# Kernel tuning notes

Hardware: AMD Instinct MI355X
Metric: run time of the kernel (lower is better)

## Reference

```python
import jax, jax.numpy as jnp
import numpy as np

B, V, C = 8192, 512, 16  # batch, num_variables, constraints per variable
N1 = V + 1  # augmented with bias column


def setup_inputs() -> dict:
    key = jax.random.key(0)
    k1, k2, k3 = jax.random.split(key, 3)
    preds = jax.random.normal(k1, (B, V), dtype=jnp.float32)
    # Acyclic structure: variable v's constraints only reference earlier
    # variables (columns < v) plus the bias column (column V).
    cols = jnp.arange(N1)[None, :]              # [1, N1]
    vids = jnp.arange(V)[:, None]               # [V, 1]
    mask = ((cols < vids) | (cols == V)).astype(jnp.float32)[:, None, :]  # [V,1,N1]
    scale = 0.1
    pos_mats = jax.random.normal(k2, (V, C, N1), dtype=jnp.float32) * scale * mask
    neg_mats = jax.random.normal(k3, (V, C, N1), dtype=jnp.float32) * scale * mask
    return {"preds": preds, "pos_mats": pos_mats, "neg_mats": neg_mats}


def reference(preds, pos_mats, neg_mats):
    # Augment preds with a ones column (bias), as in the original __call__.
    b = preds.shape[0]
    p0 = jnp.concatenate([preds, jnp.ones((b, 1), preds.dtype)], axis=1)  # [B, N1]
    var_ids = jnp.arange(pos_mats.shape[0])

    def step(p, xs):
        pm, nm, v = xs  # pm, nm: [C, N1]
        # apply_matrix: (preds * matrix).sum(-1) with max / min reduction over C
        lower = jnp.einsum('bn,cn->bc', p, pm).max(axis=1)  # [B]
        upper = jnp.einsum('bn,cn->bc', p, nm).min(axis=1)  # [B]
        # get_final_x_correction: clamp prediction into [lower, upper]
        corrected = jnp.minimum(jnp.maximum(p[:, v], lower), upper)
        p = p.at[:, v].set(corrected)
        return p, None

    pf, _ = jax.lax.scan(step, p0, (pos_mats, neg_mats, var_ids))
    return pf[:, : preds.shape[1]]
```

## Files before the change

kernel.cpp:

```cpp
#include <hip/hip_runtime.h>

#define BATCH 8192
#define V 512
#define N1 513
#define KCH 16
#define NCHUNKS 32
#define RB 32
#define NT 1024
#define PKS 520
#define SJP 772

typedef __bf16 bf16_t;
typedef bf16_t bf16x8 __attribute__((ext_vector_type(8)));
typedef float f32x4 __attribute__((ext_vector_type(4)));
typedef float f32x2 __attribute__((ext_vector_type(2)));

#define EPP 4194304ull
#define DV_OFF (EPP * 2ull)
#define BV_OFF (DV_OFF + 1048576ull)

__device__ __forceinline__ f32x4 mfma16(bf16x8 a, bf16x8 b, f32x4 c) {
    return __builtin_amdgcn_mfma_f32_16x16x32_bf16(a, b, c, 0, 0, 0);
}

__device__ __forceinline__ float bcast_lane(float x, int l) {
    return __int_as_float(__builtin_amdgcn_readlane(__float_as_int(x), l));
}

__device__ __forceinline__ float dpp_xor1_max(float x) {
    const int xi = __float_as_int(x);
    const float o = __int_as_float(
        __builtin_amdgcn_update_dpp(xi, xi, 0xB1, 0xF, 0xF, false));
    return fmaxf(x, o);
}

__global__ __launch_bounds__(256)
void repack_all(const float* __restrict__ pos, const float* __restrict__ neg,
                bf16_t* __restrict__ Mhi, float* __restrict__ Dv,
                float* __restrict__ Bv)
{
    __shared__ float bufP[256 * 17];
    __shared__ float bufN[256 * 17];
    const int bx = blockIdx.x;
    if (bx < 496) {
        const int cc  = (bx >> 4) + 1;
        const int kb  = bx & 15;
        const int nkb = (cc + 1) >> 1;
        if (kb >= nkb) return;
        const int klen = 16 * cc;
        const size_t base = 16384ull * (size_t)((cc * cc) / 4) + (size_t)kb * 16384ull;
        for (int e = threadIdx.x; e < 16384; e += 256) {
            const int t = e >> 9, s = (e >> 3) & 63, jj = e & 7;
            const int c = s & 15, q = s >> 4;
            const int v = cc * 16 + (t >> 1);
            const int k = kb * 32 + 8 * q + jj;
            const float* src = (t & 1) ? neg : pos;
            float x = (k < klen) ? src[(size_t)(v * 16 + c) * N1 + k] : 0.0f;
            if (t & 1) x = -x;
            Mhi[base + e] = (bf16_t)x;
        }
    } else {
        const int cc = bx - 496;
        for (int idx = threadIdx.x; idx < 4096; idx += 256) {
            const int r = idx >> 4, kk = idx & 15;
            const size_t row = (size_t)(cc * 256 + r);
            bufP[r * 17 + kk] = pos[row * N1 + cc * 16 + kk];
            bufN[r * 17 + kk] = neg[row * N1 + cc * 16 + kk];
        }
        __syncthreads();
        for (int idx = threadIdx.x; idx < 8192; idx += 256) {
            const int vl = idx >> 9, j = idx & 511;
            const int vlo = j >> 5, c = j & 15;
            const int m = (j >> 4) & 1;
            const float x = (m ? bufN : bufP)[(vlo * 16 + c) * 17 + vl];
            Dv[(size_t)cc * 8192 + idx] = m ? -x : x;
        }
        for (int j = threadIdx.x; j < 512; j += 256) {
            const int vlo = j >> 5, c = j & 15;
            const int m = (j >> 4) & 1;
            const float* src = m ? neg : pos;
            const float x = src[(size_t)(cc * 256 + vlo * 16 + c) * N1 + V];
            Bv[(size_t)cc * 512 + j] = m ? -x : x;
        }
    }
}

__global__ __launch_bounds__(NT, 4)
void shield_fused(const float* __restrict__ preds,
                  const bf16_t* __restrict__ Mhi,
                  const float* __restrict__ Dv, const float* __restrict__ Bv,
                  float* __restrict__ out)
{
    __shared__ bf16_t Phi[RB * PKS];
    __shared__ float  S[RB * SJP];

    const int tid  = threadIdx.x;
    const int b0   = blockIdx.x * RB;
    const int lane = tid & 63;
    const int w    = tid >> 6;
    const int cq   = lane & 15;
    const int q    = lane >> 4;
    const int rp0  = w * 2;

    {
        const int r = tid >> 5, seg = tid & 31;
        const float* prow = preds + (size_t)(b0 + r) * V + seg * 16;
        #pragma unroll
        for (int k = 0; k < 16; k += 4) {
            const float4 p4 = *(const float4*)(prow + k);
            const int n = seg * 16 + k;
            Phi[r * PKS + n + 0] = (bf16_t)p4.x;
            Phi[r * PKS + n + 1] = (bf16_t)p4.y;
            Phi[r * PKS + n + 2] = (bf16_t)p4.z;
            Phi[r * PKS + n + 3] = (bf16_t)p4.w;
        }
    }

    int tJ[2], sct[2];
    #pragma unroll
    for (int tt = 0; tt < 2; ++tt) {
        tJ[tt]  = ((2 * w + tt) << 4) + cq;
        sct[tt] = 12 * (tJ[tt] >> 3) + (tJ[tt] & 7);
    }
    const int aoff0 = cq * PKS + 8 * q;
    const int aoff1 = (16 + cq) * PKS + 8 * q;

    f32x4 acc[2][2];
    #pragma unroll
    for (int tt = 0; tt < 2; ++tt) {
        const float b = Bv[tJ[tt]];
        acc[0][tt] = f32x4{b, b, b, b};
        acc[1][tt] = f32x4{b, b, b, b};
    }

    #pragma unroll 1
    for (int cc = 0; cc < NCHUNKS; ++cc) {
        const int v0 = cc * 16;
        const int  ccn  = cc + 1;
        const bool hasN = ccn < NCHUNKS;
        const int  nkbN = hasN ? ((ccn + 1) >> 1) : 0;
        const bf16_t* phN = Mhi + 16384ull * (size_t)((ccn * ccn) / 4)
                          + (size_t)lane * 8 + (size_t)(2 * w) * 512;

        #pragma unroll
        for (int tt = 0; tt < 2; ++tt)
            #pragma unroll
            for (int reg = 0; reg < 4; ++reg) {
                S[(4 * q + reg) * SJP + sct[tt]]      = acc[0][tt][reg];
                S[(16 + 4 * q + reg) * SJP + sct[tt]] = acc[1][tt][reg];
            }
        __syncthreads();

        f32x2 s2[8];
        {
            const float* sp = &S[rp0 * SJP + 12 * lane];
            const float4 a0 = *(const float4*)(sp);
            const float4 a1 = *(const float4*)(sp + 4);
            const float4 c0 = *(const float4*)(sp + SJP);
            const float4 c1 = *(const float4*)(sp + SJP + 4);
            s2[0] = f32x2{a0.x, c0.x}; s2[1] = f32x2{a0.y, c0.y};
            s2[2] = f32x2{a0.z, c0.z}; s2[3] = f32x2{a0.w, c0.w};
            s2[4] = f32x2{a1.x, c1.x}; s2[5] = f32x2{a1.y, c1.y};
            s2[6] = f32x2{a1.z, c1.z}; s2[7] = f32x2{a1.w, c1.w};
        }

        const bf16x8 poA0 = *(const bf16x8*)(Phi + rp0 * PKS + v0);
        const bf16x8 poA1 = *(const bf16x8*)(Phi + rp0 * PKS + v0 + 8);
        const bf16x8 poB0 = *(const bf16x8*)(Phi + (rp0 + 1) * PKS + v0);
        const bf16x8 poB1 = *(const bf16x8*)(Phi + (rp0 + 1) * PKS + v0 + 8);

        if (hasN) {
            #pragma unroll
            for (int tt = 0; tt < 2; ++tt) {
                const float b = Bv[(ccn << 9) + tJ[tt]];
                acc[0][tt] = f32x4{b, b, b, b};
                acc[1][tt] = f32x4{b, b, b, b};
            }
        }

        #pragma unroll
        for (int vl = 0; vl < KCH; ++vl) {
            const int vcur = v0 + vl;
            const bool doKb = hasN && (vl < nkbN - 1);

            bf16x8 fa0, fa1, fb0, fb1;
            if (doKb) {
                const int k0 = vl * 32;
                fa0 = *(const bf16x8*)(Phi + aoff0 + k0);
                fa1 = *(const bf16x8*)(Phi + aoff1 + k0);
                const bf16_t* pb = phN + (size_t)k0 * 512;
                fb0 = *(const bf16x8*)(pb);
                fb1 = *(const bf16x8*)(pb + 512);
            }

            float dv[8];
            {
                const float* dp = Dv + ((size_t)vcur << 9) + 8 * lane;
                const float4 d0 = *(const float4*)(dp);
                const float4 d1 = *(const float4*)(dp + 4);
                dv[0]=d0.x; dv[1]=d0.y; dv[2]=d0.z; dv[3]=d0.w;
                dv[4]=d1.x; dv[5]=d1.y; dv[6]=d1.z; dv[7]=d1.w;
            }
            const float po_[2] = {
                (float)(vl < 8 ? poA0[vl & 7] : poA1[vl & 7]),
                (float)(vl < 8 ? poB0[vl & 7] : poB1[vl & 7])
            };

            float red[2];
            #pragma unroll
            for (int r = 0; r < 2; ++r) {
                const float m0 = fmaxf(fmaxf(s2[0][r], s2[1][r]), s2[2][r]);
                const float m1 = fmaxf(fmaxf(s2[3][r], s2[4][r]), s2[5][r]);
                const float m2 = fmaxf(s2[6][r], s2[7][r]);
                const float mxr = fmaxf(fmaxf(m0, m1), m2);
                red[r] = dpp_xor1_max(mxr);
            }
            float pc[2];
            #pragma unroll
            for (int r = 0; r < 2; ++r) {
                const float lw  = bcast_lane(red[r], 4 * vl);
                const float nup = bcast_lane(red[r], 4 * vl + 2);
                pc[r] = fminf(fmaxf(po_[r], lw), -nup);
            }
            if (lane == 4 * vl) {
                Phi[rp0 * PKS + vcur]       = (bf16_t)pc[0];
                Phi[(rp0 + 1) * PKS + vcur] = (bf16_t)pc[1];
            }
            const f32x2 pcv = {pc[0], pc[1]};
            #pragma unroll
            for (int jj = 0; jj < 8; ++jj) {
                const f32x2 dsp = {dv[jj], dv[jj]};
                s2[jj] = __builtin_elementwise_fma(dsp, pcv, s2[jj]);
            }

            if (doKb) {
                acc[0][0] = mfma16(fa0, fb0, acc[0][0]);
                acc[1][0] = mfma16(fa1, fb0, acc[1][0]);
                acc[0][1] = mfma16(fa0, fb1, acc[0][1]);
                acc[1][1] = mfma16(fa1, fb1, acc[1][1]);
            }
        }

        __syncthreads();

        if (hasN) {
            const int k0 = (nkbN - 1) * 32;
            const bf16x8 fa0 = *(const bf16x8*)(Phi + aoff0 + k0);
            const bf16x8 fa1 = *(const bf16x8*)(Phi + aoff1 + k0);
            const bf16_t* pb = phN + (size_t)k0 * 512;
            const bf16x8 fb0 = *(const bf16x8*)(pb);
            const bf16x8 fb1 = *(const bf16x8*)(pb + 512);
            acc[0][0] = mfma16(fa0, fb0, acc[0][0]);
            acc[1][0] = mfma16(fa1, fb0, acc[1][0]);
            acc[0][1] = mfma16(fa0, fb1, acc[0][1]);
            acc[1][1] = mfma16(fa1, fb1, acc[1][1]);
        }
    }

    {
        const int r = tid >> 5, seg = tid & 31;
        float* orow = out + (size_t)(b0 + r) * V + seg * 16;
        #pragma unroll
        for (int k = 0; k < 16; k += 4) {
            const int n = seg * 16 + k;
            float4 o;
            o.x = (float)Phi[r * PKS + n + 0];
            o.y = (float)Phi[r * PKS + n + 1];
            o.z = (float)Phi[r * PKS + n + 2];
            o.w = (float)Phi[r * PKS + n + 3];
            *(float4*)(orow + k) = o;
        }
    }
}

extern "C" void kernel_launch(void* const* d_in, const int* in_sizes, int n_in,
                              void* d_out, int out_size, void* d_ws, size_t ws_size,
                              hipStream_t stream) {
    const float* preds = (const float*)d_in[0];
    const float* pos   = (const float*)d_in[1];
    const float* neg   = (const float*)d_in[2];
    float* o = (float*)d_out;
    char* base = (char*)d_ws;
    bf16_t* Mhi = (bf16_t*)base;
    float*  Dv  = (float*)(base + DV_OFF);
    float*  Bv  = (float*)(base + BV_OFF);
    repack_all<<<dim3(528), 256, 0, stream>>>(pos, neg, Mhi, Dv, Bv);
    shield_fused<<<dim3(BATCH / RB), NT, 0, stream>>>(preds, Mhi, Dv, Bv, o);
}
```

Before: 394.2 us.

## Prefetch next-iteration operands in serial loop and stage repack through LDS

The main sequential loop now software-pipelines its global and LDS loads. The Dv row and the MFMA A/B fragments for iteration vl+1 are issued during iteration vl, so their latency overlaps the dependent clamp and reduction chain. Separately, the repack kernel first loads 32-column tiles of pos/neg into shared memory with coalesced reads, then scatters them into the bf16 MFMA layout. This replaces the previous strided global gathers. The cost is higher register pressure from the double-buffered fragments, plus a larger shared buffer in the repack kernel.

```diff
diff --git a/kernel.cpp b/kernel.cpp
--- a/kernel.cpp
+++ b/kernel.cpp
@@ -39,8 +39,7 @@
                 bf16_t* __restrict__ Mhi, float* __restrict__ Dv,
                 float* __restrict__ Bv)
 {
-    __shared__ float bufP[256 * 17];
-    __shared__ float bufN[256 * 17];
+    __shared__ float sb[2 * 256 * 33];
     const int bx = blockIdx.x;
     if (bx < 496) {
         const int cc  = (bx >> 4) + 1;
@@ -48,19 +47,32 @@
         const int nkb = (cc + 1) >> 1;
         if (kb >= nkb) return;
         const int klen = 16 * cc;
+        for (int idx = threadIdx.x; idx < 8192; idx += 256) {
+            const int r = idx >> 5, k32 = idx & 31;
+            const int k = kb * 32 + k32;
+            const size_t row = (size_t)cc * 256 + r;
+            float xp = 0.0f, xn = 0.0f;
+            if (k < klen) {
+                xp = pos[row * N1 + k];
+                xn = -neg[row * N1 + k];
+            }
+            sb[r * 33 + k32]            = xp;
+            sb[256 * 33 + r * 33 + k32] = xn;
+        }
+        __syncthreads();
         const size_t base = 16384ull * (size_t)((cc * cc) / 4) + (size_t)kb * 16384ull;
         for (int e = threadIdx.x; e < 16384; e += 256) {
             const int t = e >> 9, s = (e >> 3) & 63, jj = e & 7;
             const int c = s & 15, q = s >> 4;
-            const int v = cc * 16 + (t >> 1);
-            const int k = kb * 32 + 8 * q + jj;
-            const float* src = (t & 1) ? neg : pos;
-            float x = (k < klen) ? src[(size_t)(v * 16 + c) * N1 + k] : 0.0f;
-            if (t & 1) x = -x;
-            Mhi[base + e] = (bf16_t)x;
+            const int vloc = t >> 1, m = t & 1;
+            const int r = vloc * 16 + c;
+            const int kl = 8 * q + jj;
+            Mhi[base + e] = (bf16_t)sb[m * 256 * 33 + r * 33 + kl];
         }
     } else {
         const int cc = bx - 496;
+        float* bufP = sb;
+        float* bufN = sb + 256 * 17;
         for (int idx = threadIdx.x; idx < 4096; idx += 256) {
             const int r = idx >> 4, kk = idx & 15;
             const size_t row = (size_t)(cc * 256 + r);
@@ -178,29 +190,43 @@
             }
         }
 
+        float4 dn0, dn1;
+        {
+            const float* dp = Dv + ((size_t)v0 << 9) + 8 * lane;
+            dn0 = *(const float4*)(dp);
+            dn1 = *(const float4*)(dp + 4);
+        }
+        bf16x8 fan0, fan1, fbn0, fbn1;
+        if (hasN && 0 < nkbN - 1) {
+            fan0 = *(const bf16x8*)(Phi + aoff0);
+            fan1 = *(const bf16x8*)(Phi + aoff1);
+            fbn0 = *(const bf16x8*)(phN);
+            fbn1 = *(const bf16x8*)(phN + 512);
+        }
+
         #pragma unroll
         for (int vl = 0; vl < KCH; ++vl) {
             const int vcur = v0 + vl;
-            const bool doKb = hasN && (vl < nkbN - 1);
-
-            bf16x8 fa0, fa1, fb0, fb1;
-            if (doKb) {
-                const int k0 = vl * 32;
-                fa0 = *(const bf16x8*)(Phi + aoff0 + k0);
-                fa1 = *(const bf16x8*)(Phi + aoff1 + k0);
+            const bool doKb  = hasN && (vl < nkbN - 1);
+            const bool doKbN = hasN && (vl + 1 < nkbN - 1);
+
+            const float4 dc0 = dn0, dc1 = dn1;
+            const bf16x8 fa0 = fan0, fa1 = fan1, fb0 = fbn0, fb1 = fbn1;
+
+            if (vl + 1 < KCH) {
+                const float* dp = Dv + ((size_t)(vcur + 1) << 9) + 8 * lane;
+                dn0 = *(const float4*)(dp);
+                dn1 = *(const float4*)(dp + 4);
+            }
+            if (doKbN) {
+                const int k0 = (vl + 1) * 32;
+                fan0 = *(const bf16x8*)(Phi + aoff0 + k0);
+                fan1 = *(const bf16x8*)(Phi + aoff1 + k0);
                 const bf16_t* pb = phN + (size_t)k0 * 512;
-                fb0 = *(const bf16x8*)(pb);
-                fb1 = *(const bf16x8*)(pb + 512);
-            }
-
-            float dv[8];
-            {
-                const float* dp = Dv + ((size_t)vcur << 9) + 8 * lane;
-                const float4 d0 = *(const float4*)(dp);
-                const float4 d1 = *(const float4*)(dp + 4);
-                dv[0]=d0.x; dv[1]=d0.y; dv[2]=d0.z; dv[3]=d0.w;
-                dv[4]=d1.x; dv[5]=d1.y; dv[6]=d1.z; dv[7]=d1.w;
-            }
+                fbn0 = *(const bf16x8*)(pb);
+                fbn1 = *(const bf16x8*)(pb + 512);
+            }
+
             const float po_[2] = {
                 (float)(vl < 8 ? poA0[vl & 7] : poA1[vl & 7]),
                 (float)(vl < 8 ? poB0[vl & 7] : poB1[vl & 7])
@@ -227,10 +253,14 @@
                 Phi[(rp0 + 1) * PKS + vcur] = (bf16_t)pc[1];
             }
             const f32x2 pcv = {pc[0], pc[1]};
-            #pragma unroll
-            for (int jj = 0; jj < 8; ++jj) {
-                const f32x2 dsp = {dv[jj], dv[jj]};
-                s2[jj] = __builtin_elementwise_fma(dsp, pcv, s2[jj]);
+            {
+                const float dvv[8] = {dc0.x, dc0.y, dc0.z, dc0.w,
+                                      dc1.x, dc1.y, dc1.z, dc1.w};
+                #pragma unroll
+                for (int jj = 0; jj < 8; ++jj) {
+                    const f32x2 dsp = {dvv[jj], dvv[jj]};
+                    s2[jj] = __builtin_elementwise_fma(dsp, pcv, s2[jj]);
+                }
             }
 
             if (doKb) {
```

Measured after the change: 584.2 us. 1.48x slower.
